# Performance work log

Hardware: AMD Instinct MI355X
Metric: run time of the kernel (lower is better)

## Reference

```python
import jax, jax.numpy as jnp
import numpy as np

RES0 = 128
SCALES = [1, 2, 4, 8]
OUT_DIM = 32
PLANES = [(0, 1), (0, 2), (1, 2)]  # itertools.combinations(range(3), 2)


def _bilinear(grid, cx, cy):
    """grid: [C,H,W]; cx maps to W, cy maps to H; coords in [-1,1].
    Matches F.grid_sample(mode='bilinear', align_corners=True, padding_mode='border')."""
    C, H, W = grid.shape
    x = jnp.clip((cx + 1.0) * 0.5 * (W - 1), 0.0, W - 1)
    y = jnp.clip((cy + 1.0) * 0.5 * (H - 1), 0.0, H - 1)
    x0 = jnp.floor(x)
    y0 = jnp.floor(y)
    wx = (x - x0)[:, None]  # [N,1]
    wy = (y - y0)[:, None]
    x0i = x0.astype(jnp.int32)
    y0i = y0.astype(jnp.int32)
    x1i = jnp.minimum(x0i + 1, W - 1)
    y1i = jnp.minimum(y0i + 1, H - 1)
    g00 = grid[:, y0i, x0i].T  # [N,C]
    g01 = grid[:, y0i, x1i].T
    g10 = grid[:, y1i, x0i].T
    g11 = grid[:, y1i, x1i].T
    top = g00 * (1.0 - wx) + g01 * wx
    bot = g10 * (1.0 - wx) + g11 * wx
    return top * (1.0 - wy) + bot * wy  # [N,C]


def _interpolate_ms_features(x, ms_grids):
    feats = []
    for scale_grids in ms_grids:  # fixed 4 scales
        interp_space = 1.0
        for ci, (a, b) in enumerate(PLANES):  # fixed 3 planes
            interp_space = interp_space * _bilinear(scale_grids[ci], x[:, a], x[:, b])
        feats.append(interp_space)
    return jnp.concatenate(feats, axis=-1)  # [N, 4*OUT_DIM]


def _mlp(f, w0, w1, w2):
    h = jax.nn.relu(f @ w0)
    h = jax.nn.relu(h @ w1)
    return h @ w2  # [N,1], linear output (tcnn, bias-free)


def setup_inputs() -> dict:
    key = jax.random.key(0)
    ks = jax.random.split(key, 16)
    N = 1_000_000
    inp = {"x": jax.random.uniform(ks[0], (N, 3), jnp.float32, -1.0, 1.0)}
    i = 1
    for s, mult in enumerate(SCALES):
        R = RES0 * mult
        for p in range(3):
            # nn.init.uniform_(a=0.1, b=0.5)
            inp[f"g{s}p{p}"] = jax.random.uniform(ks[i], (OUT_DIM, R, R), jnp.float32, 0.1, 0.5)
            i += 1
    F = OUT_DIM * len(SCALES)
    inp["w0"] = jax.random.normal(ks[13], (F, 64), jnp.float32) / np.sqrt(F).astype(np.float32)
    inp["w1"] = jax.random.normal(ks[14], (64, 64), jnp.float32) / 8.0
    inp["w2"] = jax.random.normal(ks[15], (64, 1), jnp.float32) / 8.0
    return inp


def reference(x, g0p0, g0p1, g0p2, g1p0, g1p1, g1p2, g2p0, g2p1, g2p2,
              g3p0, g3p1, g3p2, w0, w1, w2):
    ms_grids = [(g0p0, g0p1, g0p2), (g1p0, g1p1, g1p2),
                (g2p0, g2p1, g2p2), (g3p0, g3p1, g3p2)]
    features = _interpolate_ms_features(x, ms_grids)
    return _mlp(features, w0, w1, w2)
```

## Files before the change

kernel.cpp:

```cpp
#include <hip/hip_runtime.h>
#include <cstddef>


typedef unsigned short ushort_t;
typedef unsigned int uint_t;
typedef __bf16 bf16x8 __attribute__((ext_vector_type(8)));
typedef float f32x4 __attribute__((ext_vector_type(4)));

#define NBUCKET 32768

struct KParams {
  const float* x;
  const void* g[12];
  const float* w0;
  const float* w1;
  const float* w2;
  const ushort_t* w0T;
  const ushort_t* w1T;
  const float* xs;
  const int* sidx;
  float* out;
  int N;
};

struct TPA {
  const float* src[12];
  ushort_t* dst[12];
};

__device__ __forceinline__ ushort_t f32_to_bf16_rne(float f) {
  uint_t u = __float_as_uint(f);
  u = (u + 0x7FFFu + ((u >> 16) & 1u)) >> 16;
  return (ushort_t)u;
}

__global__ __launch_bounds__(256) void transpose_all(TPA tp) {
  const int b = blockIdx.x;
  int s, tile;
  if (b < 256) { s = 0; tile = b; }
  else if (b < 1280) { s = 1; tile = b - 256; }
  else if (b < 5376) { s = 2; tile = b - 1280; }
  else { s = 3; tile = b - 5376; }
  const int RR = 16384 << (2 * s);
  const int k = s * 3 + blockIdx.y;
  const float* __restrict__ in = tp.src[k];
  ushort_t* __restrict__ out = tp.dst[k];

  __shared__ float tile_s[32][65];
  const int p0 = tile * 64;
  {
    const int tp_ = threadIdx.x & 63;
    const int tc = threadIdx.x >> 6;
#pragma unroll
    for (int cc = 0; cc < 8; ++cc) {
      const int c = cc * 4 + tc;
      tile_s[c][tp_] = in[(size_t)c * RR + p0 + tp_];
    }
  }
  __syncthreads();
  {
    const int c2 = threadIdx.x & 15;
    const int tq = threadIdx.x >> 4;
    uint_t* o32 = (uint_t*)out;
#pragma unroll
    for (int pp = 0; pp < 4; ++pp) {
      const int pos = pp * 16 + tq;
      const uint_t lo = f32_to_bf16_rne(tile_s[2 * c2 + 0][pos]);
      const uint_t hi = f32_to_bf16_rne(tile_s[2 * c2 + 1][pos]);
      o32[(size_t)(p0 + pos) * 16 + c2] = lo | (hi << 16);
    }
  }
}

__global__ __launch_bounds__(256) void prep_weights(
    const float* __restrict__ w0, const float* __restrict__ w1,
    ushort_t* __restrict__ w0T, ushort_t* __restrict__ w1T) {
  const int t = threadIdx.x;
  for (int i = t; i < 128 * 64; i += 256) {
    const int k = i >> 6, n = i & 63;
    w0T[n * 128 + k] = f32_to_bf16_rne(w0[i]);
  }
  for (int i = t; i < 64 * 64; i += 256) {
    const int k = i >> 6, n = i & 63;
    w1T[n * 64 + k] = f32_to_bf16_rne(w1[i]);
  }
}

__device__ __forceinline__ uint_t spread5(uint_t v) {
  return (v & 1u) | ((v & 2u) << 2) | ((v & 4u) << 4) | ((v & 8u) << 6) |
         ((v & 16u) << 8);
}
__device__ __forceinline__ uint_t morton_key(const float* __restrict__ x,
                                             int i) {
  const float a = x[3 * i + 0];
  const float b = x[3 * i + 1];
  const float c = x[3 * i + 2];
  const uint_t ua = (uint_t)fminf(fmaxf((a + 1.0f) * 16.0f, 0.0f), 31.0f);
  const uint_t ub = (uint_t)fminf(fmaxf((b + 1.0f) * 16.0f, 0.0f), 31.0f);
  const uint_t uc = (uint_t)fminf(fmaxf((c + 1.0f) * 16.0f, 0.0f), 31.0f);
  return spread5(ua) | (spread5(ub) << 1) | (spread5(uc) << 2);
}

__global__ __launch_bounds__(256) void sort_hist(const float* __restrict__ x,
                                                 uint_t* __restrict__ cnt,
                                                 ushort_t* __restrict__ key16,
                                                 int N) {
  const int i = blockIdx.x * 256 + threadIdx.x;
  if (i < N) {
    const uint_t k = morton_key(x, i);
    key16[i] = (ushort_t)k;
    atomicAdd(&cnt[k], 1u);
  }
}

__global__ __launch_bounds__(1024) void sort_scanA(uint_t* __restrict__ cnt,
                                                   uint_t* __restrict__ bsum) {
  __shared__ uint_t s[1024];
  const int t = threadIdx.x;
  const int idx = blockIdx.x * 1024 + t;
  const uint_t v = cnt[idx];
  s[t] = v;
  __syncthreads();
  for (int off = 1; off < 1024; off <<= 1) {
    uint_t u = 0;
    if (t >= off) u = s[t - off];
    __syncthreads();
    s[t] += u;
    __syncthreads();
  }
  cnt[idx] = s[t] - v;
  if (t == 1023) bsum[blockIdx.x] = s[t];
}

__global__ __launch_bounds__(256) void sort_scanB_prepw(
    uint_t* __restrict__ bsum, const float* __restrict__ w0,
    const float* __restrict__ w1, ushort_t* __restrict__ w0T,
    ushort_t* __restrict__ w1T) {
  const int t = threadIdx.x;
  if (t == 0) {
    uint_t run = 0;
#pragma unroll
    for (int i = 0; i < 32; ++i) {
      const uint_t c = bsum[i];
      bsum[i] = run;
      run += c;
    }
  }
  for (int i = t; i < 128 * 64; i += 256) {
    const int k = i >> 6, n = i & 63;
    w0T[n * 128 + k] = f32_to_bf16_rne(w0[i]);
  }
  for (int i = t; i < 64 * 64; i += 256) {
    const int k = i >> 6, n = i & 63;
    w1T[n * 64 + k] = f32_to_bf16_rne(w1[i]);
  }
}

__global__ __launch_bounds__(256) void sort_scatter(
    const float* __restrict__ x, const ushort_t* __restrict__ key16,
    uint_t* __restrict__ cnt, const uint_t* __restrict__ bsum,
    int* __restrict__ sidx, float* __restrict__ xs, int N) {
  const int i = blockIdx.x * 256 + threadIdx.x;
  if (i >= N) return;
  const uint_t key = key16[i];
  const uint_t pos = atomicAdd(&cnt[key], 1u) + bsum[key >> 10];
  sidx[pos] = i;
  xs[3 * pos + 0] = x[3 * i + 0];
  xs[3 * pos + 1] = x[3 * i + 1];
  xs[3 * pos + 2] = x[3 * i + 2];
}

template <bool SORTED>
__global__ __launch_bounds__(512, 6) void kplanes_fused_mfma(KParams P) {
  __shared__ float arena[8704];
  int4* o4s = (int4*)arena;
  float* wxs = arena + 3072;
  float* wys = arena + 3840;
  uint_t* feat32 = (uint_t*)(arena + 4608);
  float* px = arena + 4608;

  const int t = threadIdx.x;

  int bid = blockIdx.x;
  if (SORTED) {
    const int nblk = gridDim.x;
    const int q = nblk >> 3, r = nblk & 7;
    const int xcd = bid & 7, idx = bid >> 3;
    bid = (xcd < r ? xcd * (q + 1) : r * (q + 1) + (xcd - r) * q) + idx;
  }
  const int blk0 = bid * 64;

  if (SORTED) {
    if (t < 192) {
      int idx = blk0 * 3 + t;
      if (idx >= 3 * P.N) idx = 3 * P.N - 3 + (t % 3);
      px[t] = P.xs[idx];
    }
  } else {
    if (t < 192) {
      const int p = t / 3, e = t - p * 3;
      int Pi = blk0 + p;
      if (Pi >= P.N) Pi = P.N - 1;
      px[t] = P.x[3 * Pi + e];
    }
  }
  __syncthreads();

  for (int task = t; task < 768; task += 512) {
    const int pt = task & 63;
    const int sm = task >> 6;
    const int pl = sm >> 2;
    const int s = sm & 3;
    const float cx = (pl == 2) ? px[pt * 3 + 1] : px[pt * 3 + 0];
    const float cy = (pl == 0) ? px[pt * 3 + 1] : px[pt * 3 + 2];
    const int R = 128 << s;
    const float Rm1 = (float)(R - 1);
    const float u = fminf(fmaxf((cx + 1.0f) * 0.5f * Rm1, 0.0f), Rm1);
    const float v = fminf(fmaxf((cy + 1.0f) * 0.5f * Rm1, 0.0f), Rm1);
    const float fx0 = floorf(u), fy0 = floorf(v);
    const int x0 = (int)fx0, y0 = (int)fy0;
    const int x1 = min(x0 + 1, R - 1), y1 = min(y0 + 1, R - 1);
    int4 o4;
    o4.x = y0 * R + x0;
    o4.y = y0 * R + x1;
    o4.z = y1 * R + x0;
    o4.w = y1 * R + x1;
    o4s[task] = o4;
    wxs[task] = u - fx0;
    wys[task] = v - fy0;
  }
  __syncthreads();

  const int pt = t >> 3;
  const int q = t & 7;
  const int cg = q & 3;
  const int sh = q >> 2;
  uint_t* prow = feat32 + pt * 64;
  const int wxor = (pt & 7) << 2;

#define CBASE(st) (((((st) % 3) * 4) + (2 * ((st) / 3) + sh)) * 64 + pt)
#define GIDX(st) ((2 * ((st) / 3) + sh) * 3 + ((st) % 3))
#define ISSUE(O, GP, QA, QB, QC, QD)                              \
  QA = *(const uint4*)((GP) + (size_t)(O).x * 32 + cg * 8);       \
  QB = *(const uint4*)((GP) + (size_t)(O).y * 32 + cg * 8);       \
  QC = *(const uint4*)((GP) + (size_t)(O).z * 32 + cg * 8);       \
  QD = *(const uint4*)((GP) + (size_t)(O).w * 32 + cg * 8);
#define CH2(dA, dB, dC, dD, i0, i1)                                \
  {                                                                \
    float rl = __uint_as_float((dD) << 16) * w11;                  \
    rl = fmaf(__uint_as_float((dC) << 16), w10, rl);               \
    rl = fmaf(__uint_as_float((dB) << 16), w01, rl);               \
    rl = fmaf(__uint_as_float((dA) << 16), w00, rl);               \
    f[i0] *= rl;                                                   \
    float rh = __uint_as_float((dD)&0xFFFF0000u) * w11;            \
    rh = fmaf(__uint_as_float((dC)&0xFFFF0000u), w10, rh);         \
    rh = fmaf(__uint_as_float((dB)&0xFFFF0000u), w01, rh);         \
    rh = fmaf(__uint_as_float((dA)&0xFFFF0000u), w00, rh);         \
    f[i1] *= rh;                                                   \
  }

  {
    uint4 A, B, C, D, A2, B2, C2, D2;
    float wx_c, wy_c, wx_n, wy_n;
    float f[8];

    {
      const int b_ = CBASE(0);
      const int4 o = o4s[b_];
      wx_c = wxs[b_];
      wy_c = wys[b_];
      const ushort_t* gp = (const ushort_t*)P.g[GIDX(0)];
      ISSUE(o, gp, A, B, C, D)
    }

#pragma unroll
    for (int st = 0; st < 6; ++st) {
      if (st < 5) {
        const int b_ = CBASE(st + 1);
        const int4 o = o4s[b_];
        wx_n = wxs[b_];
        wy_n = wys[b_];
        const ushort_t* gp = (const ushort_t*)P.g[GIDX(st + 1)];
        ISSUE(o, gp, A2, B2, C2, D2)
      }
      if ((st % 3) == 0) {
#pragma unroll
        for (int c = 0; c < 8; ++c) f[c] = 1.0f;
      }
      {
        const float w11 = wx_c * wy_c;
        const float w10 = wy_c - w11;
        const float w01 = wx_c - w11;
        const float w00 = 1.0f - wx_c - w10;
        CH2(A.x, B.x, C.x, D.x, 0, 1)
        CH2(A.y, B.y, C.y, D.y, 2, 3)
        CH2(A.z, B.z, C.z, D.z, 4, 5)
        CH2(A.w, B.w, C.w, D.w, 6, 7)
      }
      if ((st % 3) == 2) {
        const int s = 2 * (st / 3) + sh;
        uint_t d0, d1, d2, d3;
        asm("v_cvt_pk_bf16_f32 %0, %1, %2" : "=v"(d0) : "v"(f[0]), "v"(f[1]));
        asm("v_cvt_pk_bf16_f32 %0, %1, %2" : "=v"(d1) : "v"(f[2]), "v"(f[3]));
        asm("v_cvt_pk_bf16_f32 %0, %1, %2" : "=v"(d2) : "v"(f[4]), "v"(f[5]));
        asm("v_cvt_pk_bf16_f32 %0, %1, %2" : "=v"(d3) : "v"(f[6]), "v"(f[7]));
        uint4 dv;
        dv.x = d0; dv.y = d1; dv.z = d2; dv.w = d3;
        *(uint4*)(prow + ((s * 16 + cg * 4) ^ wxor)) = dv;
      }
      A = A2; B = B2; C = C2; D = D2;
      wx_c = wx_n; wy_c = wy_n;
    }
  }
#undef CBASE
#undef GIDX
#undef ISSUE
#undef CH2
  __syncthreads();

  ushort_t* lds_h = (ushort_t*)arena;
  float(*oparts)[64] = (float(*)[64])(arena + 2048);

  const int w = __builtin_amdgcn_readfirstlane(t >> 6);
  const int mt = w & 3;
  const int nt0 = (w >> 2) << 1;
  const int ln = t & 15;
  const int lq = (t >> 4) & 3;
  const int arow = mt * 16 + ln;

  const uint_t* farow = feat32 + arow * 64;
  const int axor = (arow & 7) << 2;
  f32x4 acc0a = {0.f, 0.f, 0.f, 0.f}, acc0b = {0.f, 0.f, 0.f, 0.f};
  const ushort_t* w0a = P.w0T + (nt0 * 16 + ln) * 128 + lq * 8;
  const ushort_t* w0b = w0a + 16 * 128;
#pragma unroll
  for (int kt = 0; kt < 4; ++kt) {
    const bf16x8 aF = *(const bf16x8*)(farow + ((kt * 16 + lq * 4) ^ axor));
    const bf16x8 bFa = *(const bf16x8*)(w0a + kt * 32);
    const bf16x8 bFb = *(const bf16x8*)(w0b + kt * 32);
    acc0a = __builtin_amdgcn_mfma_f32_16x16x32_bf16(aF, bFa, acc0a, 0, 0, 0);
    acc0b = __builtin_amdgcn_mfma_f32_16x16x32_bf16(aF, bFb, acc0b, 0, 0, 0);
  }

#pragma unroll
  for (int i = 0; i < 2; ++i) {
    const f32x4 a = i ? acc0b : acc0a;
    const int col = (nt0 + i) * 16 + ln;
#pragma unroll
    for (int jj = 0; jj < 4; ++jj) {
      const float v = fmaxf(a[jj], 0.0f);
      uint_t dv;
      asm("v_cvt_pk_bf16_f32 %0, %1, %2" : "=v"(dv) : "v"(v), "v"(v));
      const int r = mt * 16 + lq * 4 + jj;
      lds_h[r * 64 + (col ^ ((r & 7) << 3))] = (ushort_t)dv;
    }
  }
  __syncthreads();

  const ushort_t* hrow = lds_h + arow * 64;
  const int hxor = (arow & 7) << 3;
  f32x4 acc1a = {0.f, 0.f, 0.f, 0.f}, acc1b = {0.f, 0.f, 0.f, 0.f};
  const ushort_t* w1a = P.w1T + (nt0 * 16 + ln) * 64 + lq * 8;
  const ushort_t* w1b = w1a + 16 * 64;
#pragma unroll
  for (int kt = 0; kt < 2; ++kt) {
    const bf16x8 aF = *(const bf16x8*)(hrow + ((kt * 32 + lq * 8) ^ hxor));
    const bf16x8 bFa = *(const bf16x8*)(w1a + kt * 32);
    const bf16x8 bFb = *(const bf16x8*)(w1b + kt * 32);
    acc1a = __builtin_amdgcn_mfma_f32_16x16x32_bf16(aF, bFa, acc1a, 0, 0, 0);
    acc1b = __builtin_amdgcn_mfma_f32_16x16x32_bf16(aF, bFb, acc1b, 0, 0, 0);
  }

  const float w2a = P.w2[nt0 * 16 + ln];
  const float w2b = P.w2[(nt0 + 1) * 16 + ln];
  float part[4];
#pragma unroll
  for (int jj = 0; jj < 4; ++jj)
    part[jj] = fmaxf(acc1a[jj], 0.f) * w2a + fmaxf(acc1b[jj], 0.f) * w2b;
#pragma unroll
  for (int jj = 0; jj < 4; ++jj) {
    part[jj] += __shfl_xor(part[jj], 1);
    part[jj] += __shfl_xor(part[jj], 2);
    part[jj] += __shfl_xor(part[jj], 4);
    part[jj] += __shfl_xor(part[jj], 8);
  }
  if (ln == 0) {
#pragma unroll
    for (int jj = 0; jj < 4; ++jj)
      oparts[w >> 2][mt * 16 + lq * 4 + jj] = part[jj];
  }
  __syncthreads();

  if (t < 64) {
    const int Po = blk0 + t;
    if (Po < P.N) {
      const float r = oparts[0][t] + oparts[1][t];
      if (SORTED)
        P.out[P.sidx[Po]] = r;
      else
        P.out[Po] = r;
    }
  }
}

__global__ __launch_bounds__(512, 8) void kplanes_fused_scalar(KParams P) {
  __shared__ float fl[64][130];
  const int t = threadIdx.x;
  const int pg = t >> 3;
  const int sub = t & 7;
  const int blk0 = blockIdx.x * 64;

  int Pi = blk0 + pg;
  if (Pi >= P.N) Pi = P.N - 1;
  const float c0 = P.x[3 * Pi + 0];
  const float c1 = P.x[3 * Pi + 1];
  const float c2 = P.x[3 * Pi + 2];

  float feat[4][4];
#pragma unroll
  for (int s = 0; s < 4; ++s)
#pragma unroll
    for (int c = 0; c < 4; ++c) feat[s][c] = 1.0f;

#pragma unroll
  for (int s = 0; s < 4; ++s) {
    const int R = 128 << s;
    const int RR = R * R;
#pragma unroll
    for (int pl = 0; pl < 3; ++pl) {
      const float cx = (pl == 2) ? c1 : c0;
      const float cy = (pl == 0) ? c1 : c2;
      const float Rm1 = (float)(R - 1);
      const float u = fminf(fmaxf((cx + 1.0f) * 0.5f * Rm1, 0.0f), Rm1);
      const float v = fminf(fmaxf((cy + 1.0f) * 0.5f * Rm1, 0.0f), Rm1);
      const float fx0 = floorf(u), fy0 = floorf(v);
      const float wx = u - fx0, wy = v - fy0;
      const int x0 = (int)fx0, y0 = (int)fy0;
      const int x1 = min(x0 + 1, R - 1), y1 = min(y0 + 1, R - 1);
      const float w11 = wx * wy;
      const float w10 = wy - w11;
      const float w01 = wx - w11;
      const float w00 = 1.0f - wx - w10;
      const float* gp = (const float*)P.g[s * 3 + pl];
      const int i00 = y0 * R + x0, i01 = y0 * R + x1;
      const int i10 = y1 * R + x0, i11 = y1 * R + x1;
#pragma unroll
      for (int c = 0; c < 4; ++c) {
        const size_t cb = (size_t)(sub * 4 + c) * RR;
        feat[s][c] *= gp[cb + i00] * w00 + gp[cb + i01] * w01 +
                      gp[cb + i10] * w10 + gp[cb + i11] * w11;
      }
    }
  }

#pragma unroll
  for (int s = 0; s < 4; ++s)
#pragma unroll
    for (int c = 0; c < 4; ++c)
      fl[pg][s * 32 + sub * 4 + c] = feat[s][c];
  __syncthreads();

  const int p = t & 63;
  const int g = __builtin_amdgcn_readfirstlane(t >> 6);

  const float* w0c = P.w0 + g * 8;
  float part[8];
#pragma unroll
  for (int jj = 0; jj < 8; ++jj) part[jj] = 0.0f;
#pragma unroll 16
  for (int k = 0; k < 128; ++k) {
    const float f = fl[p][k];
#pragma unroll
    for (int jj = 0; jj < 8; ++jj)
      part[jj] = fmaf(f, w0c[(size_t)k * 64 + jj], part[jj]);
  }
  __syncthreads();
#pragma unroll
  for (int jj = 0; jj < 8; ++jj)
    fl[p][g * 8 + jj] = fmaxf(part[jj], 0.0f);
  __syncthreads();

  const float* w1c = P.w1 + g * 8;
  float h1[8];
#pragma unroll
  for (int jj = 0; jj < 8; ++jj) h1[jj] = 0.0f;
#pragma unroll 16
  for (int k = 0; k < 64; ++k) {
    const float a = fl[p][k];
#pragma unroll
    for (int jj = 0; jj < 8; ++jj)
      h1[jj] = fmaf(a, w1c[(size_t)k * 64 + jj], h1[jj]);
  }

  const float* w2c = P.w2 + g * 8;
  float o = 0.0f;
#pragma unroll
  for (int jj = 0; jj < 8; ++jj)
    o = fmaf(fmaxf(h1[jj], 0.0f), w2c[jj], o);

  __syncthreads();
  ((float*)fl)[g * 64 + p] = o;
  __syncthreads();

  if (t < 64) {
    const int Po = blk0 + t;
    if (Po < P.N) {
      const float* f0 = (const float*)fl;
      float r = 0.0f;
#pragma unroll
      for (int j = 0; j < 8; ++j) r += f0[j * 64 + t];
      P.out[Po] = r;
    }
  }
}

extern "C" void kernel_launch(void* const* d_in, const int* in_sizes, int n_in,
                              void* d_out, int out_size, void* d_ws, size_t ws_size,
                              hipStream_t stream) {
  KParams P;
  P.x = (const float*)d_in[0];
  P.w0 = (const float*)d_in[13];
  P.w1 = (const float*)d_in[14];
  P.w2 = (const float*)d_in[15];
  P.out = (float*)d_out;
  const int N = in_sizes[0] / 3;
  P.N = N;
  P.xs = nullptr;
  P.sidx = nullptr;

  size_t need = 0;
  for (int s = 0; s < 4; ++s) {
    const size_t R = (size_t)(128 << s);
    need += 3ull * 32ull * R * R * sizeof(ushort_t);
  }
  const size_t walign = (need + 255) & ~(size_t)255;
  const size_t wbytes = (size_t)(64 * 128 + 64 * 64) * sizeof(ushort_t);
  const size_t cntoff = (walign + wbytes + 255) & ~(size_t)255;
  const size_t cntbytes = (size_t)NBUCKET * 4;
  const size_t bsumoff = cntoff + cntbytes;
  const size_t keyoff = (bsumoff + 128 + 255) & ~(size_t)255;
  const size_t sidxoff = (keyoff + (size_t)N * 2 + 255) & ~(size_t)255;
  const size_t xsoff = (sidxoff + (size_t)N * 4 + 255) & ~(size_t)255;
  const size_t total_sorted = xsoff + (size_t)N * 12;

  const int nblk = (N + 63) / 64;
  if (ws_size >= walign + wbytes) {
    ushort_t* w = (ushort_t*)d_ws;
    TPA tpa;
    size_t off = 0;
    for (int s = 0; s < 4; ++s) {
      const int R = 128 << s;
      const int RR = R * R;
      for (int pl = 0; pl < 3; ++pl) {
        tpa.src[s * 3 + pl] = (const float*)d_in[1 + s * 3 + pl];
        tpa.dst[s * 3 + pl] = w + off;
        P.g[s * 3 + pl] = w + off;
        off += (size_t)32 * RR;
      }
    }
    dim3 tg(21760, 3);
    transpose_all<<<tg, 256, 0, stream>>>(tpa);

    ushort_t* w0T = (ushort_t*)((char*)d_ws + walign);
    ushort_t* w1T = w0T + 64 * 128;
    P.w0T = w0T;
    P.w1T = w1T;

    if (ws_size >= total_sorted) {
      uint_t* cnt = (uint_t*)((char*)d_ws + cntoff);
      uint_t* bsum = (uint_t*)((char*)d_ws + bsumoff);
      ushort_t* key16 = (ushort_t*)((char*)d_ws + keyoff);
      int* sidx = (int*)((char*)d_ws + sidxoff);
      float* xs = (float*)((char*)d_ws + xsoff);
      hipMemsetAsync(cnt, 0, cntbytes, stream);
      const int pblk = (N + 255) / 256;
      sort_hist<<<pblk, 256, 0, stream>>>(P.x, cnt, key16, N);
      sort_scanA<<<32, 1024, 0, stream>>>(cnt, bsum);
      sort_scanB_prepw<<<1, 256, 0, stream>>>(bsum, P.w0, P.w1, w0T, w1T);
      sort_scatter<<<pblk, 256, 0, stream>>>(P.x, key16, cnt, bsum, sidx, xs, N);
      P.xs = xs;
      P.sidx = sidx;
      kplanes_fused_mfma<true><<<nblk, 512, 0, stream>>>(P);
    } else {
      prep_weights<<<1, 256, 0, stream>>>(P.w0, P.w1, w0T, w1T);
      kplanes_fused_mfma<false><<<nblk, 512, 0, stream>>>(P);
    }
  } else {
    for (int k = 0; k < 12; ++k) P.g[k] = (const void*)d_in[1 + k];
    P.w0T = nullptr;
    P.w1T = nullptr;
    kplanes_fused_scalar<<<nblk, 512, 0, stream>>>(P);
  }
}
```

Measured before the change: 637.0 us.

## Fuse grid transpose with sort histogram and refine Morton buckets to 18 bits

Merges the grid transpose and the Morton histogram into one launch. The transpose now uses float4 loads and uint4 stores. The two scan kernels become one, using a last-block ticket to scan the block sums, and the stored 16-bit key buffer is dropped in favour of recomputing the key during scatter. The Morton grid grows from 32^3 to 64^3 buckets for finer spatial locality in the main kernel. The aim is fewer launches and better gather locality, at the cost of a larger count array to clear and scan and more key arithmetic.

```diff
diff --git a/kernel.cpp b/kernel.cpp
--- a/kernel.cpp
+++ b/kernel.cpp
@@ -7,7 +7,8 @@
 typedef __bf16 bf16x8 __attribute__((ext_vector_type(8)));
 typedef float f32x4 __attribute__((ext_vector_type(4)));
 
-#define NBUCKET 32768
+#define NBUCKET 262144
+#define NTRANSP 65280
 
 struct KParams {
   const float* x;
@@ -34,42 +35,67 @@
   return (ushort_t)u;
 }
 
-__global__ __launch_bounds__(256) void transpose_all(TPA tp) {
+__device__ __forceinline__ uint_t spread6(uint_t v) {
+  return (v & 1u) | ((v & 2u) << 2) | ((v & 4u) << 4) | ((v & 8u) << 6) |
+         ((v & 16u) << 8) | ((v & 32u) << 10);
+}
+__device__ __forceinline__ uint_t morton_key(const float* __restrict__ x,
+                                             int i) {
+  const float a = x[3 * i + 0];
+  const float b = x[3 * i + 1];
+  const float c = x[3 * i + 2];
+  const uint_t ua = (uint_t)fminf(fmaxf((a + 1.0f) * 32.0f, 0.0f), 63.0f);
+  const uint_t ub = (uint_t)fminf(fmaxf((b + 1.0f) * 32.0f, 0.0f), 63.0f);
+  const uint_t uc = (uint_t)fminf(fmaxf((c + 1.0f) * 32.0f, 0.0f), 63.0f);
+  return spread6(ua) | (spread6(ub) << 1) | (spread6(uc) << 2);
+}
+
+__global__ __launch_bounds__(256) void front_transpose_hist(
+    TPA tp, const float* __restrict__ x, uint_t* __restrict__ cnt, int N) {
   const int b = blockIdx.x;
+  const int t = threadIdx.x;
+  if (b >= NTRANSP) {
+    const int i = (b - NTRANSP) * 256 + t;
+    if (i < N) atomicAdd(&cnt[morton_key(x, i)], 1u);
+    return;
+  }
+  const int v = b / 3;
+  const int pl = b - v * 3;
   int s, tile;
-  if (b < 256) { s = 0; tile = b; }
-  else if (b < 1280) { s = 1; tile = b - 256; }
-  else if (b < 5376) { s = 2; tile = b - 1280; }
-  else { s = 3; tile = b - 5376; }
+  if (v < 256) { s = 0; tile = v; }
+  else if (v < 1280) { s = 1; tile = v - 256; }
+  else if (v < 5376) { s = 2; tile = v - 1280; }
+  else { s = 3; tile = v - 5376; }
   const int RR = 16384 << (2 * s);
-  const int k = s * 3 + blockIdx.y;
+  const int k = s * 3 + pl;
   const float* __restrict__ in = tp.src[k];
   ushort_t* __restrict__ out = tp.dst[k];
 
-  __shared__ float tile_s[32][65];
+  __shared__ float tile_s[32][68];
   const int p0 = tile * 64;
+#pragma unroll
+  for (int it = 0; it < 2; ++it) {
+    const int idx = it * 256 + t;
+    const int row = idx >> 4;
+    const int qc = idx & 15;
+    const float4 vv = *(const float4*)(in + (size_t)row * RR + p0 + qc * 4);
+    *(float4*)&tile_s[row][qc * 4] = vv;
+  }
+  __syncthreads();
+  const int pos = t >> 2;
+  const int cq = t & 3;
+  uint4 dv;
   {
-    const int tp_ = threadIdx.x & 63;
-    const int tc = threadIdx.x >> 6;
-#pragma unroll
-    for (int cc = 0; cc < 8; ++cc) {
-      const int c = cc * 4 + tc;
-      tile_s[c][tp_] = in[(size_t)c * RR + p0 + tp_];
-    }
-  }
-  __syncthreads();
-  {
-    const int c2 = threadIdx.x & 15;
-    const int tq = threadIdx.x >> 4;
-    uint_t* o32 = (uint_t*)out;
-#pragma unroll
-    for (int pp = 0; pp < 4; ++pp) {
-      const int pos = pp * 16 + tq;
-      const uint_t lo = f32_to_bf16_rne(tile_s[2 * c2 + 0][pos]);
-      const uint_t hi = f32_to_bf16_rne(tile_s[2 * c2 + 1][pos]);
-      o32[(size_t)(p0 + pos) * 16 + c2] = lo | (hi << 16);
-    }
-  }
+    uint_t d[4];
+#pragma unroll
+    for (int h = 0; h < 4; ++h) {
+      const uint_t lo = f32_to_bf16_rne(tile_s[cq * 8 + 2 * h + 0][pos]);
+      const uint_t hi = f32_to_bf16_rne(tile_s[cq * 8 + 2 * h + 1][pos]);
+      d[h] = lo | (hi << 16);
+    }
+    dv.x = d[0]; dv.y = d[1]; dv.z = d[2]; dv.w = d[3];
+  }
+  *(uint4*)((uint_t*)out + (size_t)(p0 + pos) * 16 + cq * 4) = dv;
 }
 
 __global__ __launch_bounds__(256) void prep_weights(
@@ -86,38 +112,28 @@
   }
 }
 
-__device__ __forceinline__ uint_t spread5(uint_t v) {
-  return (v & 1u) | ((v & 2u) << 2) | ((v & 4u) << 4) | ((v & 8u) << 6) |
-         ((v & 16u) << 8);
-}
-__device__ __forceinline__ uint_t morton_key(const float* __restrict__ x,
-                                             int i) {
-  const float a = x[3 * i + 0];
-  const float b = x[3 * i + 1];
-  const float c = x[3 * i + 2];
-  const uint_t ua = (uint_t)fminf(fmaxf((a + 1.0f) * 16.0f, 0.0f), 31.0f);
-  const uint_t ub = (uint_t)fminf(fmaxf((b + 1.0f) * 16.0f, 0.0f), 31.0f);
-  const uint_t uc = (uint_t)fminf(fmaxf((c + 1.0f) * 16.0f, 0.0f), 31.0f);
-  return spread5(ua) | (spread5(ub) << 1) | (spread5(uc) << 2);
-}
-
-__global__ __launch_bounds__(256) void sort_hist(const float* __restrict__ x,
-                                                 uint_t* __restrict__ cnt,
-                                                 ushort_t* __restrict__ key16,
-                                                 int N) {
-  const int i = blockIdx.x * 256 + threadIdx.x;
-  if (i < N) {
-    const uint_t k = morton_key(x, i);
-    key16[i] = (ushort_t)k;
-    atomicAdd(&cnt[k], 1u);
-  }
-}
-
-__global__ __launch_bounds__(1024) void sort_scanA(uint_t* __restrict__ cnt,
-                                                   uint_t* __restrict__ bsum) {
+__global__ __launch_bounds__(1024) void sort_scan_prepw(
+    uint_t* __restrict__ cnt, uint_t* __restrict__ bsum,
+    uint_t* __restrict__ done, const float* __restrict__ w0,
+    const float* __restrict__ w1, ushort_t* __restrict__ w0T,
+    ushort_t* __restrict__ w1T) {
   __shared__ uint_t s[1024];
+  __shared__ uint_t ticket;
   const int t = threadIdx.x;
-  const int idx = blockIdx.x * 1024 + t;
+  const int bidx = blockIdx.x;
+
+  if (bidx == 0) {
+    for (int i = t; i < 128 * 64; i += 1024) {
+      const int k = i >> 6, n = i & 63;
+      w0T[n * 128 + k] = f32_to_bf16_rne(w0[i]);
+    }
+    for (int i = t; i < 64 * 64; i += 1024) {
+      const int k = i >> 6, n = i & 63;
+      w1T[n * 64 + k] = f32_to_bf16_rne(w1[i]);
+    }
+  }
+
+  const int idx = bidx * 1024 + t;
   const uint_t v = cnt[idx];
   s[t] = v;
   __syncthreads();
@@ -129,40 +145,35 @@
     __syncthreads();
   }
   cnt[idx] = s[t] - v;
-  if (t == 1023) bsum[blockIdx.x] = s[t];
-}
-
-__global__ __launch_bounds__(256) void sort_scanB_prepw(
-    uint_t* __restrict__ bsum, const float* __restrict__ w0,
-    const float* __restrict__ w1, ushort_t* __restrict__ w0T,
-    ushort_t* __restrict__ w1T) {
-  const int t = threadIdx.x;
-  if (t == 0) {
-    uint_t run = 0;
-#pragma unroll
-    for (int i = 0; i < 32; ++i) {
-      const uint_t c = bsum[i];
-      bsum[i] = run;
-      run += c;
-    }
-  }
-  for (int i = t; i < 128 * 64; i += 256) {
-    const int k = i >> 6, n = i & 63;
-    w0T[n * 128 + k] = f32_to_bf16_rne(w0[i]);
-  }
-  for (int i = t; i < 64 * 64; i += 256) {
-    const int k = i >> 6, n = i & 63;
-    w1T[n * 64 + k] = f32_to_bf16_rne(w1[i]);
+  if (t == 1023) bsum[bidx] = s[t];
+
+  __threadfence();
+  if (t == 0) ticket = atomicAdd(done, 1u);
+  __syncthreads();
+  if (ticket == 255) {
+    __threadfence();
+    uint_t bv = 0;
+    if (t < 256) bv = bsum[t];
+    s[t] = bv;
+    __syncthreads();
+    for (int off = 1; off < 256; off <<= 1) {
+      uint_t u = 0;
+      if (t >= off && t < 256) u = s[t - off];
+      __syncthreads();
+      if (t < 256) s[t] += u;
+      __syncthreads();
+    }
+    if (t < 256) bsum[t] = s[t] - bv;
   }
 }
 
 __global__ __launch_bounds__(256) void sort_scatter(
-    const float* __restrict__ x, const ushort_t* __restrict__ key16,
-    uint_t* __restrict__ cnt, const uint_t* __restrict__ bsum,
-    int* __restrict__ sidx, float* __restrict__ xs, int N) {
+    const float* __restrict__ x, uint_t* __restrict__ cnt,
+    const uint_t* __restrict__ bsum, int* __restrict__ sidx,
+    float* __restrict__ xs, int N) {
   const int i = blockIdx.x * 256 + threadIdx.x;
   if (i >= N) return;
-  const uint_t key = key16[i];
+  const uint_t key = morton_key(x, i);
   const uint_t pos = atomicAdd(&cnt[key], 1u) + bsum[key >> 10];
   sidx[pos] = i;
   xs[3 * pos + 0] = x[3 * i + 0];
@@ -537,13 +548,14 @@
   const size_t wbytes = (size_t)(64 * 128 + 64 * 64) * sizeof(ushort_t);
   const size_t cntoff = (walign + wbytes + 255) & ~(size_t)255;
   const size_t cntbytes = (size_t)NBUCKET * 4;
-  const size_t bsumoff = cntoff + cntbytes;
-  const size_t keyoff = (bsumoff + 128 + 255) & ~(size_t)255;
-  const size_t sidxoff = (keyoff + (size_t)N * 2 + 255) & ~(size_t)255;
+  const size_t doneoff = cntoff + cntbytes;
+  const size_t bsumoff = doneoff + 256;
+  const size_t sidxoff = (bsumoff + 1024 + 255) & ~(size_t)255;
   const size_t xsoff = (sidxoff + (size_t)N * 4 + 255) & ~(size_t)255;
   const size_t total_sorted = xsoff + (size_t)N * 12;
 
   const int nblk = (N + 63) / 64;
+  const int pblk = (N + 255) / 256;
   if (ws_size >= walign + wbytes) {
     ushort_t* w = (ushort_t*)d_ws;
     TPA tpa;
@@ -558,9 +570,6 @@
         off += (size_t)32 * RR;
       }
     }
-    dim3 tg(21760, 3);
-    transpose_all<<<tg, 256, 0, stream>>>(tpa);
-
     ushort_t* w0T = (ushort_t*)((char*)d_ws + walign);
     ushort_t* w1T = w0T + 64 * 128;
     P.w0T = w0T;
@@ -568,20 +577,20 @@
 
     if (ws_size >= total_sorted) {
       uint_t* cnt = (uint_t*)((char*)d_ws + cntoff);
+      uint_t* done = (uint_t*)((char*)d_ws + doneoff);
       uint_t* bsum = (uint_t*)((char*)d_ws + bsumoff);
-      ushort_t* key16 = (ushort_t*)((char*)d_ws + keyoff);
       int* sidx = (int*)((char*)d_ws + sidxoff);
       float* xs = (float*)((char*)d_ws + xsoff);
-      hipMemsetAsync(cnt, 0, cntbytes, stream);
-      const int pblk = (N + 255) / 256;
-      sort_hist<<<pblk, 256, 0, stream>>>(P.x, cnt, key16, N);
-      sort_scanA<<<32, 1024, 0, stream>>>(cnt, bsum);
-      sort_scanB_prepw<<<1, 256, 0, stream>>>(bsum, P.w0, P.w1, w0T, w1T);
-      sort_scatter<<<pblk, 256, 0, stream>>>(P.x, key16, cnt, bsum, sidx, xs, N);
+      hipMemsetAsync(cnt, 0, cntbytes + 256, stream);
+      front_transpose_hist<<<NTRANSP + pblk, 256, 0, stream>>>(tpa, P.x, cnt, N);
+      sort_scan_prepw<<<256, 1024, 0, stream>>>(cnt, bsum, done, P.w0, P.w1,
+                                                w0T, w1T);
+      sort_scatter<<<pblk, 256, 0, stream>>>(P.x, cnt, bsum, sidx, xs, N);
       P.xs = xs;
       P.sidx = sidx;
       kplanes_fused_mfma<true><<<nblk, 512, 0, stream>>>(P);
     } else {
+      front_transpose_hist<<<NTRANSP, 256, 0, stream>>>(tpa, P.x, nullptr, N);
       prep_weights<<<1, 256, 0, stream>>>(P.w0, P.w1, w0T, w1T);
       kplanes_fused_mfma<false><<<nblk, 512, 0, stream>>>(P);
     }
```

After: 693.0 us. +8.8%, slower.
